# Optimization experiments

Measured on AMD Instinct MI355X. Metric: run time of the kernel, lower is better.

## Reference

```python
import jax, jax.numpy as jnp
import numpy as np

B, M, D, H = 32, 1024, 768, 256


def setup_inputs() -> dict:
    key = jax.random.key(0)
    k = jax.random.split(key, 6)
    V = jax.random.normal(k[0], (B, M, D), dtype=jnp.float32)
    alpha = jnp.float32(0.5)
    # torch nn.Linear weights: [out, in]
    WV_w = jax.random.normal(k[1], (H, D), dtype=jnp.float32) * (1.0 / np.sqrt(D))
    WV_b = jnp.zeros((H,), dtype=jnp.float32)
    W_conv = jax.random.normal(k[2], (H, H), dtype=jnp.float32) * (1.0 / np.sqrt(H))
    res_w = jax.random.normal(k[3], (H, D), dtype=jnp.float32) * (1.0 / np.sqrt(D))
    res_b = jnp.zeros((H,), dtype=jnp.float32)
    return {"V": V, "alpha": alpha, "WV_w": WV_w, "WV_b": WV_b,
            "W_conv": W_conv, "res_w": res_w, "res_b": res_b}


def reference(V, alpha, WV_w, WV_b, W_conv, res_w, res_b):
    # global feature awareness enhancement: alpha*V + (1-alpha)*mean
    g = jnp.mean(V, axis=1, keepdims=True)            # [B,1,D]
    V_enh = alpha * V + (1.0 - alpha) * g             # [B,M,D]
    # projection (torch Linear: x @ W.T + b)
    Vp = jnp.einsum('bmd,hd->bmh', V_enh, WV_w) + WV_b  # [B,M,H]
    # dynamic incidence matrix: row-softmax of Vp @ Vp.T
    sim = jnp.einsum('bmh,bnh->bmn', Vp, Vp)          # [B,M,M]
    H_TV = jax.nn.softmax(sim, axis=-1)               # [B,M,M]
    # hypergraph convolution: H @ ((H.T @ X) @ W)
    t1 = jnp.einsum('bnm,bnh->bmh', H_TV, Vp)         # H.T @ X -> [B,M,H]
    t2 = jnp.einsum('bmh,hk->bmk', t1, W_conv)        # [B,M,H]
    O = jnp.einsum('bmn,bnh->bmh', H_TV, t2)          # [B,M,H]
    # residual projection + relu
    res = jnp.einsum('bmd,hd->bmh', V, res_w) + res_b  # [B,M,H]
    return jax.nn.relu(O + res)
```

## Files before the change

kernel.cpp:

```cpp
#include <hip/hip_runtime.h>
#include <math.h>


typedef __attribute__((ext_vector_type(8))) short bf16x8;
typedef __attribute__((ext_vector_type(4))) float f32x4;

__device__ __forceinline__ ushort f2b(float f) {
    unsigned u = __float_as_uint(f);
    return (ushort)((u + 0x7fffu + ((u >> 16) & 1u)) >> 16);
}
__device__ __forceinline__ float b2f(ushort u) {
    return __uint_as_float((unsigned)u << 16);
}
__device__ __forceinline__ uint4 pack8(float4 a, float4 b) {
    uint4 r;
    r.x = f2b(a.x) | ((unsigned)f2b(a.y) << 16);
    r.y = f2b(a.z) | ((unsigned)f2b(a.w) << 16);
    r.z = f2b(b.x) | ((unsigned)f2b(b.y) << 16);
    r.w = f2b(b.z) | ((unsigned)f2b(b.w) << 16);
    return r;
}

__device__ __forceinline__ void gl16(const void* g, void* l) {
    __builtin_amdgcn_global_load_lds(
        (__attribute__((address_space(1))) const unsigned*)g,
        (__attribute__((address_space(3))) unsigned*)l, 16, 0, 0);
}

__device__ __forceinline__ void gemm_core(const ushort* __restrict__ A,
                                          const ushort* __restrict__ Bt,
                                          int K, ushort* As, ushort* Bs,
                                          f32x4 acc[4][4]) {
    const int tid = threadIdx.x;
    const int lane = tid & 63;
    const int wave = tid >> 6;
    const int l8 = lane >> 3, l7 = lane & 7;
    const int swz = ((l7 ^ l8) << 4);
    const char* pa[4];
    const char* pb[4];
    ushort* la[4];
    ushort* lb[4];
    #pragma unroll
    for (int i = 0; i < 4; ++i) {
        int r = (wave * 4 + i) * 8 + l8;
        pa[i] = (const char*)A + (size_t)r * (K * 2) + swz;
        pb[i] = (const char*)Bt + (size_t)r * (K * 2) + swz;
        la[i] = As + (wave * 4 + i) * 512;
        lb[i] = Bs + (wave * 4 + i) * 512;
    }
    const int rr = lane & 15;
    const int kq = (lane >> 4) << 4;
    const int mask = (rr & 7) << 4;
    const int c0 = kq ^ mask;
    const int c1 = (64 + kq) ^ mask;
    const int wr = (wave >> 1) * 64, wc = (wave & 1) * 64;
    const int arow0 = (wr + rr) * 128, brow0 = (wc + rr) * 128;

    for (int k0 = 0; k0 < K; k0 += 64) {
        __syncthreads();
        #pragma unroll
        for (int i = 0; i < 4; ++i) {
            gl16(pa[i], la[i]);
            gl16(pb[i], lb[i]);
            pa[i] += 128; pb[i] += 128;
        }
        __syncthreads();
        #pragma unroll
        for (int ks = 0; ks < 2; ++ks) {
            const int cc = ks ? c1 : c0;
            bf16x8 av[4], bv[4];
            #pragma unroll
            for (int i = 0; i < 4; ++i) {
                av[i] = *(const bf16x8*)((const char*)As + arow0 + i * 2048 + cc);
                bv[i] = *(const bf16x8*)((const char*)Bs + brow0 + i * 2048 + cc);
            }
            #pragma unroll
            for (int i = 0; i < 4; ++i)
                #pragma unroll
                for (int j = 0; j < 4; ++j)
                    acc[i][j] = __builtin_amdgcn_mfma_f32_16x16x32_bf16(av[i], bv[j], acc[i][j], 0, 0, 0);
        }
    }
}

#define EPI_COORDS \
    const int lane = threadIdx.x & 63; \
    const int wave = threadIdx.x >> 6; \
    const int rb = (wave >> 1) * 64 + (lane >> 4) * 4; \
    const int cb = (wave & 1) * 64 + (lane & 15);

__global__ __launch_bounds__(192) void k_castmean(const float* __restrict__ V,
                                                  ushort* __restrict__ Vb,
                                                  float* __restrict__ gpart) {
    const int b = blockIdx.x, mc = blockIdx.y, t = threadIdx.x;
    const size_t base = ((size_t)(b * 1024 + mc * 64)) * 768 + t * 4;
    const float* src = V + base;
    ushort* dst = Vb + base;
    float4 s = make_float4(0.f, 0.f, 0.f, 0.f);
    for (int r = 0; r < 64; ++r) {
        float4 v = *(const float4*)(src + (size_t)r * 768);
        s.x += v.x; s.y += v.y; s.z += v.z; s.w += v.w;
        unsigned u0 = f2b(v.x) | ((unsigned)f2b(v.y) << 16);
        unsigned u1 = f2b(v.z) | ((unsigned)f2b(v.w) << 16);
        *(uint2*)(dst + (size_t)r * 768) = make_uint2(u0, u1);
    }
    *(float4*)&gpart[(size_t)(mc * 32 + b) * 768 + t * 4] = s;
}

__global__ __launch_bounds__(256) void k_gsum(const float* __restrict__ gpart, float* __restrict__ g) {
    int idx = blockIdx.x * 256 + threadIdx.x;
    float s = 0.f;
    #pragma unroll
    for (int c = 0; c < 16; ++c) s += gpart[(size_t)c * 24576 + idx];
    g[idx] = s * (1.0f / 1024.0f);
}

__global__ __launch_bounds__(256) void k_gW(const float* __restrict__ g,
                                            const float* __restrict__ WVw,
                                            float* __restrict__ gW) {
    int idx = blockIdx.x * 256 + threadIdx.x;
    int b = idx >> 8, h = idx & 255;
    const float* gr = g + b * 768;
    const float* wr = WVw + (size_t)h * 768;
    float s = 0.f;
    for (int d = 0; d < 768; ++d) s += gr[d] * wr[d];
    gW[idx] = s;
}

__global__ __launch_bounds__(256) void k_castw(const float* __restrict__ WVw,
                                               const float* __restrict__ resw,
                                               ushort* __restrict__ Wcat) {
    int id = blockIdx.x * 256 + threadIdx.x;
    int n = id / 96, c = (id - n * 96) * 8;
    const float* src = (n < 256) ? (WVw + (size_t)n * 768 + c) : (resw + (size_t)(n - 256) * 768 + c);
    *(uint4*)(Wcat + (size_t)n * 768 + c) = pack8(*(const float4*)src, *(const float4*)(src + 4));
}

__global__ __launch_bounds__(256) void k_wct(const float* __restrict__ Wc, ushort* __restrict__ WcT) {
    __shared__ float t[64][65];
    const int r0 = blockIdx.y * 64, c0 = blockIdx.x * 64;
    const int tid = threadIdx.x;
    #pragma unroll
    for (int i = 0; i < 4; ++i) {
        int r = (tid >> 4) + i * 16, c4 = (tid & 15) * 4;
        float4 v = *(const float4*)&Wc[(size_t)(r0 + r) * 256 + c0 + c4];
        t[r][c4] = v.x; t[r][c4 + 1] = v.y; t[r][c4 + 2] = v.z; t[r][c4 + 3] = v.w;
    }
    __syncthreads();
    #pragma unroll
    for (int i = 0; i < 4; ++i) {
        int oc = (tid >> 4) + i * 16, r4 = (tid & 15) * 4;
        unsigned lo = f2b(t[r4][oc]) | ((unsigned)f2b(t[r4 + 1][oc]) << 16);
        unsigned hi = f2b(t[r4 + 2][oc]) | ((unsigned)f2b(t[r4 + 3][oc]) << 16);
        *(uint2*)&WcT[(size_t)(c0 + oc) * 256 + r0 + r4] = make_uint2(lo, hi);
    }
}

__global__ __launch_bounds__(256) void k_proj(const ushort* __restrict__ Vb, const ushort* __restrict__ Wcat,
                                              const float* __restrict__ WVb, const float* __restrict__ resb,
                                              const float* __restrict__ gW, const float* __restrict__ alpha_p,
                                              ushort* __restrict__ Vp, ushort* __restrict__ resv) {
    __shared__ ushort As[128 * 64], Bs[128 * 64];
    f32x4 acc[4][4] = {};
    const int j = (blockIdx.x & 7) * 128 + (blockIdx.x >> 3);
    const int n0 = (j & 3) * 128, m0 = (j >> 2) * 128;
    gemm_core(Vb + (size_t)m0 * 768, Wcat + (size_t)n0 * 768, 768, As, Bs, acc);
    EPI_COORDS
    const float alpha = *alpha_p, oma = 1.0f - alpha;
    #pragma unroll
    for (int i = 0; i < 4; ++i)
        #pragma unroll
        for (int jj = 0; jj < 4; ++jj) {
            int gcol = n0 + cb + jj * 16;
            #pragma unroll
            for (int r = 0; r < 4; ++r) {
                int grow = m0 + rb + i * 16 + r;
                float v = acc[i][jj][r];
                if (gcol < 256) {
                    float o = alpha * v + oma * gW[((grow >> 10) << 8) + gcol] + WVb[gcol];
                    Vp[(size_t)grow * 256 + gcol] = f2b(o);
                } else {
                    resv[(size_t)grow * 256 + gcol - 256] = f2b(v + resb[gcol - 256]);
                }
            }
        }
}

__global__ __launch_bounds__(256) void k_rownorm(const ushort* __restrict__ Vp, float* __restrict__ rn) {
    const int row = blockIdx.x * 4 + (threadIdx.x >> 6);
    const int lane = threadIdx.x & 63;
    uint2 v = *(const uint2*)(Vp + (size_t)row * 256 + lane * 4);
    float f0 = b2f((ushort)(v.x & 0xffff)), f1 = b2f((ushort)(v.x >> 16));
    float f2 = b2f((ushort)(v.y & 0xffff)), f3 = b2f((ushort)(v.y >> 16));
    float s = f0 * f0 + f1 * f1 + f2 * f2 + f3 * f3;
    #pragma unroll
    for (int o = 32; o > 0; o >>= 1) s += __shfl_xor(s, o, 64);
    if (lane == 0) rn[row] = s;
}

__global__ __launch_bounds__(256) void k_shift(const float* __restrict__ rn, float* __restrict__ shift) {
    const int b = blockIdx.x, tid = threadIdx.x;
    const float* p = rn + b * 1024;
    float m = fmaxf(fmaxf(p[tid], p[tid + 256]), fmaxf(p[tid + 512], p[tid + 768]));
    #pragma unroll
    for (int o = 32; o > 0; o >>= 1) m = fmaxf(m, __shfl_xor(m, o, 64));
    __shared__ float red[4];
    if ((tid & 63) == 0) red[tid >> 6] = m;
    __syncthreads();
    if (tid == 0)
        shift[b] = fmaxf(fmaxf(red[0], red[1]), fmaxf(red[2], red[3]));
}

__global__ __launch_bounds__(256) void k_sim(const ushort* __restrict__ Vp,
                                             const float* __restrict__ shift,
                                             ushort* __restrict__ E,
                                             float* __restrict__ Z) {
    __shared__ ushort As[128 * 64], Bs[128 * 64];
    f32x4 acc[4][4] = {};
    const int j = (blockIdx.x & 7) * 256 + (blockIdx.x >> 3);
    const int n0 = (j & 7) * 128, m0 = ((j >> 3) & 7) * 128, b = j >> 6;
    const ushort* Vb_ = Vp + (size_t)b * 1024 * 256;
    gemm_core(Vb_ + (size_t)m0 * 256, Vb_ + (size_t)n0 * 256, 256, As, Bs, acc);
    ushort* Eb = E + ((size_t)b << 20);
    const float sh = shift[b];
    EPI_COORDS
    #pragma unroll
    for (int i = 0; i < 4; ++i)
        #pragma unroll
        for (int r = 0; r < 4; ++r) {
            const int row = m0 + rb + i * 16 + r;
            float e[4];
            float s = 0.f;
            #pragma unroll
            for (int jj = 0; jj < 4; ++jj) {
                e[jj] = __expf(acc[i][jj][r] - sh);
                s += e[jj];
                Eb[(size_t)row * 1024 + n0 + cb + jj * 16] = f2b(e[jj]);
            }
            s += __shfl_xor(s, 1, 64);
            s += __shfl_xor(s, 2, 64);
            s += __shfl_xor(s, 4, 64);
            s += __shfl_xor(s, 8, 64);
            if ((lane & 15) == 0)
                atomicAdd(&Z[b * 1024 + row], s);
        }
}

__global__ __launch_bounds__(256) void k_trbs(const ushort* __restrict__ Vp,
                                              const float* __restrict__ Z,
                                              ushort* __restrict__ VpZT) {
    __shared__ ushort t[64][68];
    const int b = blockIdx.z;
    const ushort* ib = Vp + (size_t)b * 1024 * 256;
    ushort* ob = VpZT + (size_t)b * 256 * 1024;
    const int c0 = blockIdx.x * 64, r0 = blockIdx.y * 64;
    const int tid = threadIdx.x;
    #pragma unroll
    for (int i = 0; i < 4; ++i) {
        int r = (tid >> 4) + i * 16, c4 = (tid & 15) * 4;
        uint2 v = *(const uint2*)(ib + (size_t)(r0 + r) * 256 + c0 + c4);
        float iz = 1.0f / Z[b * 1024 + r0 + r];
        unsigned lo = f2b(b2f((ushort)(v.x & 0xffff)) * iz) |
                      ((unsigned)f2b(b2f((ushort)(v.x >> 16)) * iz) << 16);
        unsigned hi = f2b(b2f((ushort)(v.y & 0xffff)) * iz) |
                      ((unsigned)f2b(b2f((ushort)(v.y >> 16)) * iz) << 16);
        *(uint2*)&t[r][c4] = make_uint2(lo, hi);
    }
    __syncthreads();
    #pragma unroll
    for (int i = 0; i < 4; ++i) {
        int oc = (tid >> 4) + i * 16, r4 = (tid & 15) * 4;
        unsigned lo = t[r4][oc] | ((unsigned)t[r4 + 1][oc] << 16);
        unsigned hi = t[r4 + 2][oc] | ((unsigned)t[r4 + 3][oc] << 16);
        *(uint2*)(ob + (size_t)(c0 + oc) * 1024 + r0 + r4) = make_uint2(lo, hi);
    }
}

__global__ __launch_bounds__(512) void k_t12(const ushort* __restrict__ E,
                                             const ushort* __restrict__ VpZT,
                                             const ushort* __restrict__ WcT,
                                             ushort* __restrict__ t2T) {
    __shared__ char smem[65536];
    char* Asb = smem;
    char* Bsb = smem + 16384;

    const int j = (blockIdx.x & 7) * 32 + (blockIdx.x >> 3);
    const int m0 = (j & 7) * 128;
    const int b = j >> 3;
    const ushort* Eb = E + ((size_t)b << 20) + (size_t)m0 * 1024;
    const ushort* Vz = VpZT + (size_t)b * 256 * 1024;
    const int tid = threadIdx.x;
    const int lane = tid & 63, wave = tid >> 6;
    const int l8 = lane >> 3, l7 = lane & 7;
    const int swz = (l7 ^ l8) << 4;

    const char* pa[2]; char* la[2];
    const char* pb[4]; char* lb[4];
    #pragma unroll
    for (int ii = 0; ii < 2; ++ii) {
        int r = wave * 16 + ii * 8 + l8;
        pa[ii] = (const char*)(Eb + (size_t)r * 1024) + swz;
        la[ii] = Asb + (wave * 16 + ii * 8) * 128;
    }
    #pragma unroll
    for (int ii = 0; ii < 4; ++ii) {
        int r = wave * 32 + ii * 8 + l8;
        pb[ii] = (const char*)(Vz + (size_t)r * 1024) + swz;
        lb[ii] = Bsb + (wave * 32 + ii * 8) * 128;
    }
    const int rr = lane & 15;
    const int kq = (lane >> 4) << 4;
    const int mask = (rr & 7) << 4;
    const int wr = (wave >> 2) * 64, wc = (wave & 3) * 64;
    f32x4 acc[4][4] = {};
    for (int k0 = 0; k0 < 1024; k0 += 64) {
        __syncthreads();
        #pragma unroll
        for (int ii = 0; ii < 2; ++ii) { gl16(pa[ii], la[ii]); pa[ii] += 128; }
        #pragma unroll
        for (int ii = 0; ii < 4; ++ii) { gl16(pb[ii], lb[ii]); pb[ii] += 128; }
        __syncthreads();
        #pragma unroll
        for (int ks = 0; ks < 2; ++ks) {
            const int cc = (ks * 64 + kq) ^ mask;
            bf16x8 av[4], bv[4];
            #pragma unroll
            for (int i = 0; i < 4; ++i) {
                av[i] = *(const bf16x8*)(Asb + (wr + i * 16 + rr) * 128 + cc);
                bv[i] = *(const bf16x8*)(Bsb + (wc + i * 16 + rr) * 128 + cc);
            }
            #pragma unroll
            for (int i = 0; i < 4; ++i)
                #pragma unroll
                for (int jj = 0; jj < 4; ++jj)
                    acc[i][jj] = __builtin_amdgcn_mfma_f32_16x16x32_bf16(av[i], bv[jj], acc[i][jj], 0, 0, 0);
        }
    }
    __syncthreads();
    const int rb = wr + (lane >> 4) * 4;
    const int cbh = wc + (lane & 15);
    #pragma unroll
    for (int i = 0; i < 4; ++i)
        #pragma unroll
        for (int jj = 0; jj < 4; ++jj) {
            int h = cbh + jj * 16;
            #pragma unroll
            for (int r = 0; r < 4; ++r) {
                int m = rb + i * 16 + r;
                *(ushort*)(smem + m * 512 + ((2 * h) ^ ((m & 7) << 4))) = f2b(acc[i][jj][r]);
            }
        }
    __syncthreads();
    f32x4 acc2[4][4] = {};
    #pragma unroll
    for (int k2 = 0; k2 < 4; ++k2) {
        #pragma unroll
        for (int ks = 0; ks < 2; ++ks) {
            const int cbyte = k2 * 128 + ks * 64 + kq;
            bf16x8 av[4], bv[4];
            #pragma unroll
            for (int i = 0; i < 4; ++i) {
                int m = wr + i * 16 + rr;
                av[i] = *(const bf16x8*)(smem + m * 512 + (cbyte ^ ((m & 7) << 4)));
                int h = wc + i * 16 + rr;
                bv[i] = *(const bf16x8*)((const char*)WcT + h * 512 + cbyte);
            }
            #pragma unroll
            for (int i = 0; i < 4; ++i)
                #pragma unroll
                for (int jj = 0; jj < 4; ++jj)
                    acc2[i][jj] = __builtin_amdgcn_mfma_f32_16x16x32_bf16(av[i], bv[jj], acc2[i][jj], 0, 0, 0);
        }
    }
    __syncthreads();
    #pragma unroll
    for (int i = 0; i < 4; ++i)
        #pragma unroll
        for (int jj = 0; jj < 4; ++jj) {
            int h = cbh + jj * 16;
            int m = rb + i * 16;
            unsigned u0 = f2b(acc2[i][jj][0]) | ((unsigned)f2b(acc2[i][jj][1]) << 16);
            unsigned u1 = f2b(acc2[i][jj][2]) | ((unsigned)f2b(acc2[i][jj][3]) << 16);
            *(uint2*)(smem + h * 256 + ((2 * m) ^ ((h & 7) << 4))) = make_uint2(u0, u1);
        }
    __syncthreads();
    ushort* ob = t2T + (size_t)b * 256 * 1024 + m0;
    const int h = tid >> 1, mh = (tid & 1) * 64;
    #pragma unroll
    for (int i = 0; i < 8; ++i) {
        uint4 v = *(const uint4*)(smem + h * 256 + (((mh + i * 8) * 2) ^ ((h & 7) << 4)));
        *(uint4*)(ob + (size_t)h * 1024 + mh + i * 8) = v;
    }
}

__global__ __launch_bounds__(256) void k_O(const ushort* __restrict__ E, const ushort* __restrict__ t2T,
                                           const ushort* __restrict__ resv, const float* __restrict__ Z,
                                           float* __restrict__ out) {
    __shared__ ushort As[128 * 64], Bs[128 * 64];
    f32x4 acc[4][4] = {};
    const int j = (blockIdx.x & 7) * 64 + (blockIdx.x >> 3);
    const int n0 = (j & 1) * 128, m0 = ((j >> 1) & 7) * 128, b = j >> 4;
    gemm_core(E + ((size_t)b << 20) + (size_t)m0 * 1024,
              t2T + (size_t)b * 256 * 1024 + (size_t)n0 * 1024, 1024, As, Bs, acc);
    EPI_COORDS
    #pragma unroll
    for (int i = 0; i < 4; ++i)
        #pragma unroll
        for (int jj = 0; jj < 4; ++jj)
            #pragma unroll
            for (int r = 0; r < 4; ++r) {
                int row = m0 + rb + i * 16 + r;
                float iz = 1.0f / Z[b * 1024 + row];
                size_t off = ((size_t)(b * 1024 + row)) * 256 + n0 + cb + jj * 16;
                out[off] = fmaxf(acc[i][jj][r] * iz + b2f(resv[off]), 0.0f);
            }
}

extern "C" void kernel_launch(void* const* d_in, const int* in_sizes, int n_in,
                              void* d_out, int out_size, void* d_ws, size_t ws_size,
                              hipStream_t stream) {
    const float* V     = (const float*)d_in[0];
    const float* alpha = (const float*)d_in[1];
    const float* WVw   = (const float*)d_in[2];
    const float* WVb   = (const float*)d_in[3];
    const float* Wc    = (const float*)d_in[4];
    const float* resw  = (const float*)d_in[5];
    const float* resb  = (const float*)d_in[6];
    float* out = (float*)d_out;

    char* W = (char*)d_ws;
    ushort* Vb   = (ushort*)(W);
    ushort* E    = (ushort*)(W + (48ull  << 20));
    ushort* Vp   = (ushort*)(W + (112ull << 20));
    ushort* resv = (ushort*)(W + (128ull << 20));
    ushort* VpZT = (ushort*)(W + (144ull << 20));
    ushort* t2T  = (ushort*)(W + (192ull << 20));
    ushort* Wcat = (ushort*)(W + (208ull << 20));
    ushort* WcT  = (ushort*)(W + (209ull << 20));
    float*  gpart= (float*) (W + (210ull << 20));
    float*  g    = (float*) (W + (212ull << 20));
    float*  gW   = (float*) (W + (212ull << 20) + (128u << 10));
    float*  shv  = (float*) (W + (212ull << 20) + (256u << 10));
    float*  rn   = (float*) (W + (212ull << 20) + (512u << 10));
    float*  Z    = (float*) (W + (213ull << 20));

    hipMemsetAsync(Z, 0, 32768 * sizeof(float), stream);

    k_castmean<<<dim3(32, 16), 192, 0, stream>>>(V, Vb, gpart);
    k_gsum<<<96, 256, 0, stream>>>(gpart, g);
    k_gW<<<32, 256, 0, stream>>>(g, WVw, gW);
    k_castw<<<192, 256, 0, stream>>>(WVw, resw, Wcat);
    k_wct<<<dim3(4, 4), 256, 0, stream>>>(Wc, WcT);
    k_proj<<<1024, 256, 0, stream>>>(Vb, Wcat, WVb, resb, gW, alpha, Vp, resv);
    k_rownorm<<<8192, 256, 0, stream>>>(Vp, rn);
    k_shift<<<32, 256, 0, stream>>>(rn, shv);
    k_sim<<<2048, 256, 0, stream>>>(Vp, shv, E, Z);
    k_trbs<<<dim3(4, 16, 32), 256, 0, stream>>>(Vp, Z, VpZT);
    k_t12<<<256, 512, 0, stream>>>(E, VpZT, WcT, t2T);
    k_O<<<512, 256, 0, stream>>>(E, t2T, resv, Z, out);
}
```

Before: 384.8 us.

## Double-buffer LDS tiles in gemm_core to overlap global loads with MFMA

Splits the shared-memory staging into two ping-pong buffers so the next 64-wide K tile is loaded via global_load_lds while MFMAs consume the current tile, reducing barriers per step. Intended to hide global memory latency in all GEMM kernels. Doubles LDS per block, which lowers the number of resident blocks per CU, and the benefit depends on the compiler not inserting full waits on outstanding loads before the barrier.

```diff
diff --git a/kernel.cpp b/kernel.cpp
--- a/kernel.cpp
+++ b/kernel.cpp
@@ -29,7 +29,9 @@
 
 __device__ __forceinline__ void gemm_core(const ushort* __restrict__ A,
                                           const ushort* __restrict__ Bt,
-                                          int K, ushort* As, ushort* Bs,
+                                          int K,
+                                          ushort* As0, ushort* Bs0,
+                                          ushort* As1, ushort* Bs1,
                                           f32x4 acc[4][4]) {
     const int tid = threadIdx.x;
     const int lane = tid & 63;
@@ -38,15 +40,13 @@
     const int swz = ((l7 ^ l8) << 4);
     const char* pa[4];
     const char* pb[4];
-    ushort* la[4];
-    ushort* lb[4];
+    int lo[4];
     #pragma unroll
     for (int i = 0; i < 4; ++i) {
         int r = (wave * 4 + i) * 8 + l8;
         pa[i] = (const char*)A + (size_t)r * (K * 2) + swz;
         pb[i] = (const char*)Bt + (size_t)r * (K * 2) + swz;
-        la[i] = As + (wave * 4 + i) * 512;
-        lb[i] = Bs + (wave * 4 + i) * 512;
+        lo[i] = (wave * 4 + i) * 512;
     }
     const int rr = lane & 15;
     const int kq = (lane >> 4) << 4;
@@ -56,31 +56,34 @@
     const int wr = (wave >> 1) * 64, wc = (wave & 1) * 64;
     const int arow0 = (wr + rr) * 128, brow0 = (wc + rr) * 128;
 
-    for (int k0 = 0; k0 < K; k0 += 64) {
+#define STAGE_TO(Abuf, Bbuf) \
+    { _Pragma("unroll") for (int i = 0; i < 4; ++i) { \
+        gl16(pa[i], (Abuf) + lo[i]); gl16(pb[i], (Bbuf) + lo[i]); \
+        pa[i] += 128; pb[i] += 128; } }
+
+#define COMPUTE_ON(Abuf, Bbuf) \
+    { _Pragma("unroll") for (int ks = 0; ks < 2; ++ks) { \
+        const int cc = ks ? c1 : c0; \
+        bf16x8 av[4], bv[4]; \
+        _Pragma("unroll") for (int i = 0; i < 4; ++i) { \
+            av[i] = *(const bf16x8*)((const char*)(Abuf) + arow0 + i * 2048 + cc); \
+            bv[i] = *(const bf16x8*)((const char*)(Bbuf) + brow0 + i * 2048 + cc); } \
+        _Pragma("unroll") for (int i = 0; i < 4; ++i) \
+            _Pragma("unroll") for (int j = 0; j < 4; ++j) \
+                acc[i][j] = __builtin_amdgcn_mfma_f32_16x16x32_bf16(av[i], bv[j], acc[i][j], 0, 0, 0); } }
+
+    STAGE_TO(As0, Bs0);
+    __syncthreads();
+    for (int k0 = 0; k0 < K; k0 += 128) {
+        if (k0 + 64 < K) STAGE_TO(As1, Bs1);
+        COMPUTE_ON(As0, Bs0);
         __syncthreads();
-        #pragma unroll
-        for (int i = 0; i < 4; ++i) {
-            gl16(pa[i], la[i]);
-            gl16(pb[i], lb[i]);
-            pa[i] += 128; pb[i] += 128;
-        }
+        if (k0 + 128 < K) STAGE_TO(As0, Bs0);
+        COMPUTE_ON(As1, Bs1);
         __syncthreads();
-        #pragma unroll
-        for (int ks = 0; ks < 2; ++ks) {
-            const int cc = ks ? c1 : c0;
-            bf16x8 av[4], bv[4];
-            #pragma unroll
-            for (int i = 0; i < 4; ++i) {
-                av[i] = *(const bf16x8*)((const char*)As + arow0 + i * 2048 + cc);
-                bv[i] = *(const bf16x8*)((const char*)Bs + brow0 + i * 2048 + cc);
-            }
-            #pragma unroll
-            for (int i = 0; i < 4; ++i)
-                #pragma unroll
-                for (int j = 0; j < 4; ++j)
-                    acc[i][j] = __builtin_amdgcn_mfma_f32_16x16x32_bf16(av[i], bv[j], acc[i][j], 0, 0, 0);
-        }
-    }
+    }
+#undef STAGE_TO
+#undef COMPUTE_ON
 }
 
 #define EPI_COORDS \
@@ -88,6 +91,10 @@
     const int wave = threadIdx.x >> 6; \
     const int rb = (wave >> 1) * 64 + (lane >> 4) * 4; \
     const int cb = (wave & 1) * 64 + (lane & 15);
+
+#define GEMM_LDS \
+    __shared__ ushort As0[128 * 64], Bs0[128 * 64]; \
+    __shared__ ushort As1[128 * 64], Bs1[128 * 64];
 
 __global__ __launch_bounds__(192) void k_castmean(const float* __restrict__ V,
                                                   ushort* __restrict__ Vb,
@@ -160,11 +167,11 @@
                                               const float* __restrict__ WVb, const float* __restrict__ resb,
                                               const float* __restrict__ gW, const float* __restrict__ alpha_p,
                                               ushort* __restrict__ Vp, ushort* __restrict__ resv) {
-    __shared__ ushort As[128 * 64], Bs[128 * 64];
+    GEMM_LDS
     f32x4 acc[4][4] = {};
     const int j = (blockIdx.x & 7) * 128 + (blockIdx.x >> 3);
     const int n0 = (j & 3) * 128, m0 = (j >> 2) * 128;
-    gemm_core(Vb + (size_t)m0 * 768, Wcat + (size_t)n0 * 768, 768, As, Bs, acc);
+    gemm_core(Vb + (size_t)m0 * 768, Wcat + (size_t)n0 * 768, 768, As0, Bs0, As1, Bs1, acc);
     EPI_COORDS
     const float alpha = *alpha_p, oma = 1.0f - alpha;
     #pragma unroll
@@ -215,12 +222,12 @@
                                              const float* __restrict__ shift,
                                              ushort* __restrict__ E,
                                              float* __restrict__ Z) {
-    __shared__ ushort As[128 * 64], Bs[128 * 64];
+    GEMM_LDS
     f32x4 acc[4][4] = {};
     const int j = (blockIdx.x & 7) * 256 + (blockIdx.x >> 3);
     const int n0 = (j & 7) * 128, m0 = ((j >> 3) & 7) * 128, b = j >> 6;
     const ushort* Vb_ = Vp + (size_t)b * 1024 * 256;
-    gemm_core(Vb_ + (size_t)m0 * 256, Vb_ + (size_t)n0 * 256, 256, As, Bs, acc);
+    gemm_core(Vb_ + (size_t)m0 * 256, Vb_ + (size_t)n0 * 256, 256, As0, Bs0, As1, Bs1, acc);
     ushort* Eb = E + ((size_t)b << 20);
     const float sh = shift[b];
     EPI_COORDS
@@ -396,12 +403,12 @@
 __global__ __launch_bounds__(256) void k_O(const ushort* __restrict__ E, const ushort* __restrict__ t2T,
                                            const ushort* __restrict__ resv, const float* __restrict__ Z,
                                            float* __restrict__ out) {
-    __shared__ ushort As[128 * 64], Bs[128 * 64];
+    GEMM_LDS
     f32x4 acc[4][4] = {};
     const int j = (blockIdx.x & 7) * 64 + (blockIdx.x >> 3);
     const int n0 = (j & 1) * 128, m0 = ((j >> 1) & 7) * 128, b = j >> 4;
     gemm_core(E + ((size_t)b << 20) + (size_t)m0 * 1024,
-              t2T + (size_t)b * 256 * 1024 + (size_t)n0 * 1024, 1024, As, Bs, acc);
+              t2T + (size_t)b * 256 * 1024 + (size_t)n0 * 1024, 1024, As0, Bs0, As1, Bs1, acc);
     EPI_COORDS
     #pragma unroll
     for (int i = 0; i < 4; ++i)
```

After: 394.7 us. 2.6% more time.

## Exploit symmetry of Vp·Vpᵀ to compute only upper-triangular sim tiles

Applied to the files above, without the earlier changes.

The similarity matrix is symmetric, so k_sim now launches only the 36 upper-triangular 128x128 tiles per batch instead of all 64. Each off-diagonal tile writes its exp values for both (m,n) and, after a transpose through swizzled shared memory, (n,m), and adds column sums into Z for the mirrored rows. This cuts the GEMM work for the sim stage by about 44%, but the E write traffic stays the same and there are extra LDS transposes, syncs and atomics.

```diff
diff --git a/kernel.cpp b/kernel.cpp
--- a/kernel.cpp
+++ b/kernel.cpp
@@ -215,12 +215,17 @@
                                              const float* __restrict__ shift,
                                              ushort* __restrict__ E,
                                              float* __restrict__ Z) {
-    __shared__ ushort As[128 * 64], Bs[128 * 64];
+    __shared__ ushort smem[16384];
     f32x4 acc[4][4] = {};
-    const int j = (blockIdx.x & 7) * 256 + (blockIdx.x >> 3);
-    const int n0 = (j & 7) * 128, m0 = ((j >> 3) & 7) * 128, b = j >> 6;
+    const int jlin = (blockIdx.x & 7) * 144 + (blockIdx.x >> 3);
+    const int b = jlin / 36;
+    int idx = jlin - b * 36;
+    int ti = 0;
+    while (idx >= 8 - ti) { idx -= 8 - ti; ++ti; }
+    const int tj = ti + idx;
+    const int m0 = ti * 128, n0 = tj * 128;
     const ushort* Vb_ = Vp + (size_t)b * 1024 * 256;
-    gemm_core(Vb_ + (size_t)m0 * 256, Vb_ + (size_t)n0 * 256, 256, As, Bs, acc);
+    gemm_core(Vb_ + (size_t)m0 * 256, Vb_ + (size_t)n0 * 256, 256, smem, smem + 8192, acc);
     ushort* Eb = E + ((size_t)b << 20);
     const float sh = shift[b];
     EPI_COORDS
@@ -229,13 +234,13 @@
         #pragma unroll
         for (int r = 0; r < 4; ++r) {
             const int row = m0 + rb + i * 16 + r;
-            float e[4];
             float s = 0.f;
             #pragma unroll
             for (int jj = 0; jj < 4; ++jj) {
-                e[jj] = __expf(acc[i][jj][r] - sh);
-                s += e[jj];
-                Eb[(size_t)row * 1024 + n0 + cb + jj * 16] = f2b(e[jj]);
+                float e = __expf(acc[i][jj][r] - sh);
+                acc[i][jj][r] = e;
+                s += e;
+                Eb[(size_t)row * 1024 + n0 + cb + jj * 16] = f2b(e);
             }
             s += __shfl_xor(s, 1, 64);
             s += __shfl_xor(s, 2, 64);
@@ -244,6 +249,41 @@
             if ((lane & 15) == 0)
                 atomicAdd(&Z[b * 1024 + row], s);
         }
+    if (ti != tj) {
+        __syncthreads();
+        #pragma unroll
+        for (int i = 0; i < 4; ++i)
+            #pragma unroll
+            for (int jj = 0; jj < 4; ++jj) {
+                const int col = cb + jj * 16;
+                unsigned u0 = f2b(acc[i][jj][0]) | ((unsigned)f2b(acc[i][jj][1]) << 16);
+                unsigned u1 = f2b(acc[i][jj][2]) | ((unsigned)f2b(acc[i][jj][3]) << 16);
+                *(uint2*)((char*)smem + col * 256 + ((2 * (rb + i * 16)) ^ ((col & 7) << 4))) =
+                    make_uint2(u0, u1);
+            }
+        #pragma unroll
+        for (int jj = 0; jj < 4; ++jj) {
+            float cs = 0.f;
+            #pragma unroll
+            for (int i = 0; i < 4; ++i)
+                #pragma unroll
+                for (int r = 0; r < 4; ++r) cs += acc[i][jj][r];
+            cs += __shfl_xor(cs, 16, 64);
+            cs += __shfl_xor(cs, 32, 64);
+            if (lane < 16)
+                atomicAdd(&Z[b * 1024 + n0 + cb + jj * 16], cs);
+        }
+        __syncthreads();
+        const int tid = threadIdx.x;
+        const int c = tid >> 1, half = tid & 1;
+        ushort* orow = Eb + (size_t)(n0 + c) * 1024 + m0 + half * 64;
+        #pragma unroll
+        for (int k = 0; k < 8; ++k) {
+            uint4 v = *(const uint4*)((const char*)smem + c * 256 +
+                                      (((half * 64 + k * 8) * 2) ^ ((c & 7) << 4)));
+            *(uint4*)(orow + k * 8) = v;
+        }
+    }
 }
 
 __global__ __launch_bounds__(256) void k_trbs(const ushort* __restrict__ Vp,
@@ -454,7 +494,7 @@
     k_proj<<<1024, 256, 0, stream>>>(Vb, Wcat, WVb, resb, gW, alpha, Vp, resv);
     k_rownorm<<<8192, 256, 0, stream>>>(Vp, rn);
     k_shift<<<32, 256, 0, stream>>>(rn, shv);
-    k_sim<<<2048, 256, 0, stream>>>(Vp, shv, E, Z);
+    k_sim<<<1152, 256, 0, stream>>>(Vp, shv, E, Z);
     k_trbs<<<dim3(4, 16, 32), 256, 0, stream>>>(Vp, Z, VpZT);
     k_t12<<<256, 512, 0, stream>>>(E, VpZT, WcT, t2T);
     k_O<<<512, 256, 0, stream>>>(E, t2T, resv, Z, out);
```

Measured after the change: 381.4 us. No clear change (-0.9%).
